# Performance work log

Hardware: AMD Instinct MI355X
Metric: run time of the kernel (lower is better)

## Reference

```python
import jax, jax.numpy as jnp
import numpy as np

B, S, HID, H, D = 2, 2048, 2048, 16, 128
ROPE_THETA = 10000.0
NEG = -1e9


def _rope_tables(seq_len, dim, theta):
    inv_freq = 1.0 / (theta ** (jnp.arange(0, dim, 2, dtype=jnp.float32) / dim))
    t = jnp.arange(seq_len, dtype=jnp.float32)
    freqs = jnp.outer(t, inv_freq)                 # [S, D/2]
    emb = jnp.concatenate([freqs, freqs], axis=-1)  # [S, D]
    return jnp.cos(emb), jnp.sin(emb)


def _rotate_half(x):
    x1, x2 = jnp.split(x, 2, axis=-1)
    return jnp.concatenate([-x2, x1], axis=-1)


def setup_inputs() -> dict:
    key = jax.random.key(0)
    ks = jax.random.split(key, 12)
    hidden_states = jax.random.normal(ks[0], (B, S, HID), dtype=jnp.float32)
    Wq = jax.random.normal(ks[1], (HID, HID), dtype=jnp.float32) * 0.02
    Wk = jax.random.normal(ks[2], (HID, HID), dtype=jnp.float32) * 0.02
    Wv = jax.random.normal(ks[3], (HID, HID), dtype=jnp.float32) * 0.02
    Wo = jax.random.normal(ks[4], (HID, HID), dtype=jnp.float32) * 0.02
    bq = jnp.zeros((HID,), jnp.float32)
    bk = jnp.zeros((HID,), jnp.float32)
    bv = jnp.zeros((HID,), jnp.float32)
    beta = jax.random.normal(ks[5], (1,), dtype=jnp.float32)
    M = jax.random.normal(ks[6], (H, D, D), dtype=jnp.float32) * 0.01
    z = jax.random.uniform(ks[7], (H, D), dtype=jnp.float32) + 1.0  # strictly positive normalizer
    causal = jnp.tril(jnp.ones((S, S), dtype=bool))
    attention_mask = jnp.broadcast_to(
        jnp.where(causal, 0.0, NEG).astype(jnp.float32)[None, None], (B, 1, S, S)
    ) + jnp.zeros((B, 1, S, S), jnp.float32)
    position_ids = jnp.broadcast_to(jnp.arange(S, dtype=jnp.int32), (B, S))
    return {
        "hidden_states": hidden_states, "Wq": Wq, "bq": bq, "Wk": Wk, "bk": bk,
        "Wv": Wv, "bv": bv, "Wo": Wo, "beta": beta, "M": M, "z": z,
        "attention_mask": attention_mask, "position_ids": position_ids,
    }


def reference(hidden_states, Wq, bq, Wk, bk, Wv, bv, Wo, beta, M, z,
              attention_mask, position_ids):
    bsz, seq, hid = hidden_states.shape
    h, d = M.shape[0], M.shape[1]

    # projections (weights stored [in, out])
    q = (hidden_states @ Wq + bq).reshape(bsz, seq, h, d).transpose(0, 2, 1, 3)  # [b,h,s,d]
    k = (hidden_states @ Wk + bk).reshape(bsz, seq, h, d).transpose(0, 2, 1, 3)
    v = (hidden_states @ Wv + bv).reshape(bsz, seq, h, d).transpose(0, 2, 1, 3)

    # RoPE
    cos, sin = _rope_tables(seq, d, ROPE_THETA)          # [s, d]
    cos = cos[position_ids][:, None]                      # [b,1,s,d]
    sin = sin[position_ids][:, None]
    q = q * cos + _rotate_half(q) * sin
    k = k * cos + _rotate_half(k) * sin

    sigma = lambda x: jax.nn.elu(x) + 1.0
    sig_q = sigma(q)
    sig_k = sigma(k)

    # compressive-memory retrieval (uses pre-update M, z)
    mem_num = jnp.einsum('bhsd,hde->bhse', sig_q, M)
    mem_den = jnp.einsum('bhsd,hd->bhs', sig_q, z)
    memory_output = mem_num / mem_den[..., None]

    # memory update via outer products of feature-mapped keys and values
    M_new = M + jnp.einsum('bhsd,bhse->hde', sig_k, v)
    z_new = z + sig_k.sum(axis=(0, 2))

    # local causal attention
    scores = jnp.einsum('bhqd,bhkd->bhqk', q, k) / jnp.sqrt(jnp.float32(d))
    scores = scores + attention_mask
    attn = jax.nn.softmax(scores, axis=-1)
    attn_output = jnp.einsum('bhqk,bhkd->bhqd', attn, v)

    # gated long-term injection
    g = jax.nn.sigmoid(beta)[0]
    combined = g * memory_output + (1.0 - g) * attn_output

    combined = combined.transpose(0, 2, 1, 3).reshape(bsz, seq, h * d)
    final_output = combined @ Wo
    return (final_output, M_new, z_new)
```

## Files before the change

### kernel.cpp

```cpp
#include <hip/hip_runtime.h>


typedef float  floatx4 __attribute__((ext_vector_type(4)));
typedef __bf16 bf16x8  __attribute__((ext_vector_type(8)));

#define DEV __device__ __forceinline__

constexpr int BN  = 2;
constexpr int SS  = 2048;
constexpr int HID = 2048;
constexpr int NH  = 16;
constexpr int DD  = 128;
constexpr int BS  = BN * SS;

DEV unsigned short f2bf(float f) {
  unsigned int u = __float_as_uint(f);
  u += 0x7FFFu + ((u >> 16) & 1u);
  return (unsigned short)(u >> 16);
}
DEV float bf2f(unsigned short h) {
  return __uint_as_float(((unsigned int)h) << 16);
}
DEV float sigma_f(float x) { return x > 0.f ? x + 1.f : __expf(x); }

DEV void cp16(const unsigned short* g, unsigned short* l) {
  __builtin_amdgcn_global_load_lds(
      (const __attribute__((address_space(1))) unsigned int*)g,
      (__attribute__((address_space(3))) unsigned int*)l, 16, 0, 0);
}

DEV bf16x8 scale8(bf16x8 x, float s) {
  bf16x8 r;
  #pragma unroll
  for (int i = 0; i < 8; i++) r[i] = (__bf16)((float)x[i] * s);
  return r;
}

DEV floatx4 mfma16(bf16x8 a, bf16x8 b, floatx4 c) {
  return __builtin_amdgcn_mfma_f32_16x16x32_bf16(a, b, c, 0, 0, 0);
}

constexpr size_t WS_WOT   = 0;
constexpr size_t WS_HSB   = WS_WOT   + (size_t)HID * HID * 2;
constexpr size_t WS_WQT   = WS_HSB   + (size_t)BS  * HID * 2;
constexpr size_t WS_WKT   = WS_WQT   + (size_t)HID * HID * 2;
constexpr size_t WS_WVT   = WS_WKT   + (size_t)HID * HID * 2;
constexpr size_t WS_QB    = WS_WVT   + (size_t)HID * HID * 2;
constexpr size_t WS_KB    = WS_QB    + (size_t)BS  * HID * 2;
constexpr size_t WS_VB    = WS_KB    + (size_t)BS  * HID * 2;
constexpr size_t WS_VTB   = WS_VB    + (size_t)BS  * HID * 2;
constexpr size_t WS_ATT   = WS_VTB   + (size_t)BS  * HID * 2;
constexpr size_t WS_COMB  = WS_ATT   + (size_t)BS  * HID * 2;
constexpr size_t WS_MPART = WS_COMB  + (size_t)BS  * HID * 2;
constexpr size_t WS_ZPART = WS_MPART + (size_t)16 * NH * DD * DD * 4;
constexpr size_t WS_MTB   = WS_ZPART + (size_t)16 * NH * DD * 4;

__global__ __launch_bounds__(256) void k_prep(const float* __restrict__ hs,
                                              const float* __restrict__ Wq, const float* __restrict__ Wk,
                                              const float* __restrict__ Wv, const float* __restrict__ Wo,
                                              const float* __restrict__ M,
                                              unsigned short* __restrict__ hsb,
                                              unsigned short* tq, unsigned short* tk,
                                              unsigned short* tv, unsigned short* to_,
                                              unsigned short* __restrict__ mtb) {
  __shared__ float tile[64][65];
  const int tid = threadIdx.x;
  if (blockIdx.z == 5) {
    if (blockIdx.y >= 16 || blockIdx.x >= 4) return;
    int h = blockIdx.y;
    int d0 = (blockIdx.x & 1) * 64, e0 = (blockIdx.x >> 1) * 64;
    const float* Mh = M + (size_t)h * DD * DD;
    #pragma unroll
    for (int i = 0; i < 16; i++) {
      int idx = i * 256 + tid; int r = idx >> 6, c = idx & 63;
      tile[r][c] = Mh[(size_t)(d0 + r) * DD + e0 + c];
    }
    __syncthreads();
    #pragma unroll
    for (int i = 0; i < 16; i++) {
      int idx = i * 256 + tid; int r = idx >> 6, c = idx & 63;
      mtb[((size_t)h * DD + e0 + r) * DD + d0 + c] = f2bf(tile[c][r]);
    }
    return;
  }
  if (blockIdx.z == 4) {
    int cid = blockIdx.y * 32 + blockIdx.x;
    const float4* src = (const float4*)hs;
    ushort4* dst = (ushort4*)hsb;
    #pragma unroll
    for (int i = 0; i < 8; i++) {
      int idx = cid * 2048 + i * 256 + tid;
      float4 v = src[idx];
      ushort4 o; o.x = f2bf(v.x); o.y = f2bf(v.y); o.z = f2bf(v.z); o.w = f2bf(v.w);
      dst[idx] = o;
    }
    return;
  }
  const float* W; unsigned short* T;
  switch (blockIdx.z) {
    case 0:  W = Wq; T = tq; break;
    case 1:  W = Wk; T = tk; break;
    case 2:  W = Wv; T = tv; break;
    default: W = Wo; T = to_; break;
  }
  int k0 = blockIdx.y * 64, n0 = blockIdx.x * 64;
  #pragma unroll
  for (int i = 0; i < 16; i++) {
    int idx = i * 256 + tid; int r = idx >> 6, c = idx & 63;
    tile[r][c] = W[(size_t)(k0 + r) * HID + n0 + c];
  }
  __syncthreads();
  #pragma unroll
  for (int i = 0; i < 16; i++) {
    int idx = i * 256 + tid; int r = idx >> 6, c = idx & 63;
    T[(size_t)(n0 + r) * HID + k0 + c] = f2bf(tile[c][r]);
  }
}

constexpr int GBM = 256, GBN = 128, GBK = 32;
constexpr int NTK = HID / GBK;
constexpr int A_U    = GBM * GBK;
constexpr int SLOT_U = (GBM + GBN) * GBK;

DEV void stage_slot(const unsigned short* __restrict__ X,
                    const unsigned short* __restrict__ Wt,
                    unsigned short* slot, int m0, int n0, int k0, int tid) {
  #pragma unroll
  for (int i = 0; i < 2; i++) {
    int c = i * 512 + tid;
    int q = c >> 3, p = c & 7, t = p ^ (q & 7);
    int row = 2 * q + (t >> 2), col = k0 + ((t & 3) << 3);
    cp16(X + (size_t)(m0 + row) * HID + col, slot + c * 8);
  }
  {
    int c = tid;
    int q = c >> 3, p = c & 7, t = p ^ (q & 7);
    int row = 2 * q + (t >> 2), col = k0 + ((t & 3) << 3);
    cp16(Wt + (size_t)(n0 + row) * HID + col, slot + A_U + c * 8);
  }
}

DEV bf16x8 ldfrag(const unsigned short* base, int r, int grp) {
  int q = r >> 1;
  int p = (((r & 1) << 2) | grp) ^ (q & 7);
  return __builtin_bit_cast(bf16x8, *(const uint4*)(base + q * 64 + p * 8));
}

DEV void gemm_core(const unsigned short* __restrict__ X,
                   const unsigned short* __restrict__ Wt,
                   unsigned short* lds, int m0, int n0, floatx4 acc[4][4]) {
  const int tid = threadIdx.x;
  const int lane = tid & 63, w = tid >> 6;
  const int grp = lane >> 4, l16 = lane & 15;
  const int wm = (w >> 1) * 64, wn = (w & 1) * 64;
  #pragma unroll
  for (int i = 0; i < 4; i++)
    #pragma unroll
    for (int j = 0; j < 4; j++) acc[i][j] = floatx4{0.f, 0.f, 0.f, 0.f};
  stage_slot(X, Wt, lds,          m0, n0, 0,   tid);
  stage_slot(X, Wt, lds + SLOT_U, m0, n0, GBK, tid);
  int sl_r = 0, sl_w = 2;
  for (int t = 0; t < NTK; t++) {
    if (t + 1 < NTK) asm volatile("s_waitcnt vmcnt(3)" ::: "memory");
    else             asm volatile("s_waitcnt vmcnt(0)" ::: "memory");
    __builtin_amdgcn_s_barrier();
    asm volatile("" ::: "memory");
    if (t + 2 < NTK)
      stage_slot(X, Wt, lds + sl_w * SLOT_U, m0, n0, (t + 2) * GBK, tid);
    const unsigned short* As = lds + sl_r * SLOT_U;
    const unsigned short* Bs = As + A_U;
    bf16x8 af[4], bfr[4];
    #pragma unroll
    for (int mi = 0; mi < 4; mi++) af[mi]  = ldfrag(As, wm + mi * 16 + l16, grp);
    #pragma unroll
    for (int ni = 0; ni < 4; ni++) bfr[ni] = ldfrag(Bs, wn + ni * 16 + l16, grp);
    __builtin_amdgcn_s_setprio(1);
    #pragma unroll
    for (int mi = 0; mi < 4; mi++)
      #pragma unroll
      for (int ni = 0; ni < 4; ni++)
        acc[mi][ni] = mfma16(af[mi], bfr[ni], acc[mi][ni]);
    __builtin_amdgcn_s_setprio(0);
    asm volatile("" ::: "memory");
    sl_r = (sl_r == 2) ? 0 : sl_r + 1;
    sl_w = (sl_w == 2) ? 0 : sl_w + 1;
  }
}

__global__ __launch_bounds__(512, 4) void k_gemm_qkv(
    const unsigned short* __restrict__ Xb,
    const unsigned short* __restrict__ Wtq, const unsigned short* __restrict__ Wtk,
    const unsigned short* __restrict__ Wtv,
    const float* __restrict__ bq, const float* __restrict__ bk, const float* __restrict__ bv,
    unsigned short* __restrict__ qb, unsigned short* __restrict__ kb,
    unsigned short* __restrict__ vtb) {
  const unsigned short* Wt; const float* bias; unsigned short* out;
  switch (blockIdx.z) {
    case 0:  Wt = Wtq; bias = bq; out = qb; break;
    case 1:  Wt = Wtk; bias = bk; out = kb; break;
    default: Wt = Wtv; bias = bv; out = nullptr; break;
  }
  __shared__ __align__(16) unsigned short lds[3 * SLOT_U];
  int lin = blockIdx.y * 16 + blockIdx.x;
  lin = (lin & 7) * 32 + (lin >> 3);
  int m0 = (lin >> 4) * GBM, n0 = (lin & 15) * GBN;
  floatx4 acc[4][4];
  gemm_core(Xb, Wt, lds, m0, n0, acc);
  const int tid = threadIdx.x;
  const int lane = tid & 63, w = tid >> 6;
  const int grp = lane >> 4, l16 = lane & 15;
  const int wm = (w >> 1) * 64, wn = (w & 1) * 64;
  if (blockIdx.z == 2) {
    #pragma unroll
    for (int mi = 0; mi < 4; mi++) {
      int gr0 = m0 + wm + mi * 16;
      int bi  = gr0 >> 11;
      int ssb = (gr0 & 2047) + grp * 4;
      #pragma unroll
      for (int ni = 0; ni < 4; ni++) {
        int col = n0 + wn + ni * 16 + l16;
        float bb_ = bias[col];
        int hh = col >> 7, dd = col & 127;
        ushort4 pk;
        unsigned short* pv = (unsigned short*)&pk;
        #pragma unroll
        for (int r = 0; r < 4; r++) pv[r] = f2bf(acc[mi][ni][r] + bb_);
        *(ushort4*)(vtb + (((size_t)(bi * NH + hh)) * DD + dd) * SS + ssb) = pk;
      }
    }
    return;
  }
  __syncthreads();
  unsigned short* T = lds;
  #pragma unroll
  for (int mi = 0; mi < 4; mi++) {
    #pragma unroll
    for (int ni = 0; ni < 4; ni++) {
      int col = wn + ni * 16 + l16;
      float bb_ = bias[n0 + col];
      #pragma unroll
      for (int r = 0; r < 4; r++)
        T[(wm + mi * 16 + grp * 4 + r) * 144 + col] = f2bf(acc[mi][ni][r] + bb_);
    }
  }
  __syncthreads();
  const int hh = n0 >> 7;
  #pragma unroll
  for (int j = 0; j < 4; j++) {
    int r = j * 64 + (tid >> 3);
    int c0 = (tid & 7) * 8;
    int grow = m0 + r;
    int bi = grow >> 11, s = grow & 2047;
    bf16x8 x1 = __builtin_bit_cast(bf16x8, *(const uint4*)(T + r * 144 + c0));
    bf16x8 x2 = __builtin_bit_cast(bf16x8, *(const uint4*)(T + r * 144 + c0 + 64));
    unsigned short o1[8], o2[8];
    #pragma unroll
    for (int jj = 0; jj < 8; jj++) {
      float ang = (float)s * __expf(-(float)(c0 + jj) * (9.210340371976184f / 64.f));
      float sn, cs;
      __sincosf(ang, &sn, &cs);
      float a1 = (float)x1[jj], a2 = (float)x2[jj];
      o1[jj] = f2bf(a1 * cs - a2 * sn);
      o2[jj] = f2bf(a2 * cs + a1 * sn);
    }
    size_t base = ((size_t)(bi * NH + hh) * SS + s) * DD;
    *(uint4*)(out + base + c0)      = *(const uint4*)o1;
    *(uint4*)(out + base + c0 + 64) = *(const uint4*)o2;
  }
}

__global__ __launch_bounds__(512, 4) void k_gemm_out(const unsigned short* __restrict__ Xb,
                                                     const unsigned short* __restrict__ Wt,
                                                     float* __restrict__ outf) {
  __shared__ __align__(16) unsigned short lds[3 * SLOT_U];
  int lin = blockIdx.y * 16 + blockIdx.x;
  lin = (lin & 7) * 32 + (lin >> 3);
  int m0 = (lin >> 4) * GBM, n0 = (lin & 15) * GBN;
  floatx4 acc[4][4];
  gemm_core(Xb, Wt, lds, m0, n0, acc);
  const int lane = threadIdx.x & 63, w = threadIdx.x >> 6;
  const int grp = lane >> 4, l16 = lane & 15;
  const int wm = (w >> 1) * 64, wn = (w & 1) * 64;
  #pragma unroll
  for (int mi = 0; mi < 4; mi++)
    #pragma unroll
    for (int ni = 0; ni < 4; ni++) {
      int col = n0 + wn + ni * 16 + l16;
      #pragma unroll
      for (int r = 0; r < 4; r++) {
        int gr = m0 + wm + mi * 16 + grp * 4 + r;
        outf[(size_t)gr * HID + col] = acc[mi][ni][r];
      }
    }
}

DEV void stage_kv(const unsigned short* __restrict__ Kg,
                  const unsigned short* __restrict__ Vg,
                  unsigned short* Klb, unsigned short* Vtlb, int tid) {
  #pragma unroll
  for (int i = 0; i < 4; i++) {
    int c = i * 256 + tid;
    int kv = c >> 4, ck = c & 15;
    cp16(Kg + kv * DD + ((ck ^ (kv & 7)) << 3), Klb + c * 8);
    int dvt = c >> 3, cv = c & 7;
    cp16(Vg + (size_t)dvt * SS + ((cv ^ (dvt & 7)) << 3), Vtlb + c * 8);
  }
}

DEV void attn_update(const unsigned short* Kl, const unsigned short* Vtl,
                     unsigned short* Plw, const bf16x8* qf, floatx4* o,
                     floatx4* lacc, bool diag, int grp, int l16, int wrow) {
  const int swk = l16 & 7;
  floatx4 sacc[4];
  #pragma unroll
  for (int j = 0; j < 4; j++) sacc[j] = floatx4{0.f, 0.f, 0.f, 0.f};
  __builtin_amdgcn_s_setprio(1);
  #pragma unroll
  for (int ks = 0; ks < 4; ks++)
    #pragma unroll
    for (int j = 0; j < 4; j++) {
      bf16x8 kf = __builtin_bit_cast(bf16x8,
          *(const uint4*)(Kl + (j * 16 + l16) * 128 + (((ks * 4 + grp) ^ swk) << 3)));
      sacc[j] = __builtin_amdgcn_mfma_f32_16x16x32_bf16(qf[ks], kf, sacc[j], 0, 0, 0);
    }
  __builtin_amdgcn_s_setprio(0);
  #pragma unroll
  for (int j = 0; j < 4; j++)
    #pragma unroll
    for (int r = 0; r < 4; r++) {
      float p = (diag && (j * 16 + l16) > (wrow + grp * 4 + r)) ? 0.f : __expf(sacc[j][r]);
      Plw[(j >> 1) * 640 + (grp * 4 + r) * 40 + (j & 1) * 16 + l16] = f2bf(p);
    }
  const bf16x8 ones = __builtin_bit_cast(bf16x8,
      uint4{0x3F803F80u, 0x3F803F80u, 0x3F803F80u, 0x3F803F80u});
  __builtin_amdgcn_s_setprio(1);
  #pragma unroll
  for (int ks2 = 0; ks2 < 2; ks2++) {
    bf16x8 pf = __builtin_bit_cast(bf16x8,
        *(const uint4*)(Plw + ks2 * 640 + l16 * 40 + grp * 8));
    *lacc = __builtin_amdgcn_mfma_f32_16x16x32_bf16(pf, ones, *lacc, 0, 0, 0);
    #pragma unroll
    for (int n = 0; n < 8; n++) {
      bf16x8 vf = __builtin_bit_cast(bf16x8,
          *(const uint4*)(Vtl + (n * 16 + l16) * 64 + (((ks2 * 4 + grp) ^ swk) << 3)));
      o[n] = __builtin_amdgcn_mfma_f32_16x16x32_bf16(pf, vf, o[n], 0, 0, 0);
    }
  }
  __builtin_amdgcn_s_setprio(0);
}

__global__ __launch_bounds__(256) void k_attn(const unsigned short* __restrict__ qb,
                                              const unsigned short* __restrict__ kb,
                                              const unsigned short* __restrict__ vtb,
                                              unsigned short* __restrict__ attb) {
  const int t = blockIdx.x, bh = blockIdx.y;
  const int qtA = t, qtB = 31 - t;
  const int tid = threadIdx.x, w = tid >> 6, lane = tid & 63;
  const int grp = lane >> 4, l16 = lane & 15;
  const unsigned short* Q  = qb  + (size_t)bh * SS * DD;
  const unsigned short* K  = kb  + (size_t)bh * SS * DD;
  const unsigned short* VT = vtb + (size_t)bh * DD * SS;
  __shared__ __align__(16) unsigned short Kl[2][64 * 128];
  __shared__ __align__(16) unsigned short Vtl[2][128 * 64];
  __shared__ __align__(16) unsigned short Pl[4][1280];
  const float sc = 0.08838834764831845f;
  bf16x8 qfA[4], qfB[4];
  {
    int qrA = qtA * 64 + w * 16 + l16, qrB = qtB * 64 + w * 16 + l16;
    #pragma unroll
    for (int ks = 0; ks < 4; ks++) {
      qfA[ks] = scale8(__builtin_bit_cast(bf16x8, *(const uint4*)(Q + (size_t)qrA * DD + ks * 32 + grp * 8)), sc);
      qfB[ks] = scale8(__builtin_bit_cast(bf16x8, *(const uint4*)(Q + (size_t)qrB * DD + ks * 32 + grp * 8)), sc);
    }
  }
  floatx4 oA[8], oB[8];
  #pragma unroll
  for (int n = 0; n < 8; n++) { oA[n] = floatx4{0,0,0,0}; oB[n] = floatx4{0,0,0,0}; }
  floatx4 laccA = floatx4{0,0,0,0}, laccB = floatx4{0,0,0,0};
  stage_kv(K, VT, Kl[0], Vtl[0], tid);
  asm volatile("s_waitcnt vmcnt(0)" ::: "memory");
  __builtin_amdgcn_s_barrier();
  int cur = 0;
  for (int kt = 0; kt <= qtB; kt++) {
    asm volatile("" ::: "memory");
    if (kt < qtB)
      stage_kv(K + (size_t)(kt + 1) * 64 * DD, VT + (size_t)(kt + 1) * 64,
               Kl[cur ^ 1], Vtl[cur ^ 1], tid);
    attn_update(Kl[cur], Vtl[cur], Pl[w], qfB, oB, &laccB, kt == qtB, grp, l16, w * 16);
    if (kt <= qtA)
      attn_update(Kl[cur], Vtl[cur], Pl[w], qfA, oA, &laccA, kt == qtA, grp, l16, w * 16);
    asm volatile("" ::: "memory");
    if (kt < qtB) {
      asm volatile("s_waitcnt vmcnt(0)" ::: "memory");
      __builtin_amdgcn_s_barrier();
    }
    cur ^= 1;
  }
  #pragma unroll
  for (int r = 0; r < 4; r++) {
    float invA = 1.f / laccA[r], invB = 1.f / laccB[r];
    int rA = qtA * 64 + w * 16 + grp * 4 + r;
    int rB = qtB * 64 + w * 16 + grp * 4 + r;
    #pragma unroll
    for (int n = 0; n < 8; n++) {
      attb[(size_t)bh * SS * DD + (size_t)rA * DD + n * 16 + l16] = f2bf(oA[n][r] * invA);
      attb[(size_t)bh * SS * DD + (size_t)rB * DD + n * 16 + l16] = f2bf(oB[n][r] * invB);
    }
  }
}

__global__ __launch_bounds__(256) void k_memcomb(const unsigned short* __restrict__ qb,
                                                 const unsigned short* __restrict__ mtb,
                                                 const float* __restrict__ z,
                                                 const float* __restrict__ beta,
                                                 const unsigned short* __restrict__ attb,
                                                 unsigned short* __restrict__ comb) {
  const int st = blockIdx.x, bh = blockIdx.y;
  const int b = bh >> 4, h = bh & 15;
  const int tid = threadIdx.x, w = tid >> 6, lane = tid & 63;
  const int grp = lane >> 4, l16 = lane & 15;
  const int s0 = st * 64;
  __shared__ __align__(16) unsigned short qtl[64 * 128];
  __shared__ __align__(16) unsigned short sqt[64 * 128];
  __shared__ float zf[128];
  __shared__ float den[64];
  #pragma unroll
  for (int i = 0; i < 4; i++) {
    int c = i * 256 + tid;
    int row = c >> 4, ch = c & 15;
    cp16(qb + ((size_t)bh * SS + s0 + row) * DD + ch * 8, qtl + c * 8);
  }
  if (tid < 32) {
    #pragma unroll
    for (int j = 0; j < 4; j++) zf[tid * 4 + j] = z[h * DD + tid * 4 + j];
  }
  asm volatile("s_waitcnt vmcnt(0)" ::: "memory");
  __syncthreads();
  #pragma unroll
  for (int i = 0; i < 4; i++) {
    int c = i * 256 + tid;
    int row = c >> 4, ch = c & 15;
    bf16x8 v = __builtin_bit_cast(bf16x8, *(const uint4*)(qtl + c * 8));
    unsigned short o8[8];
    float dp = 0.f;
    #pragma unroll
    for (int j = 0; j < 8; j++) {
      float sgv = sigma_f((float)v[j]);
      dp += sgv * zf[ch * 8 + j];
      o8[j] = f2bf(sgv);
    }
    *(uint4*)(sqt + ((size_t)row * 128 + (size_t)(ch ^ (row & 15)) * 8)) =
        *(const uint4*)o8;
    #pragma unroll
    for (int msk = 1; msk < 16; msk <<= 1) dp += __shfl_xor(dp, msk, 64);
    if (l16 == 0) den[row] = dp;
  }
  __syncthreads();
  floatx4 acc[4][2];
  #pragma unroll
  for (int mi = 0; mi < 4; mi++)
    #pragma unroll
    for (int ni = 0; ni < 2; ni++) acc[mi][ni] = floatx4{0.f, 0.f, 0.f, 0.f};
  const unsigned short* Mh = mtb + (size_t)h * DD * DD;
  #pragma unroll
  for (int k = 0; k < 4; k++) {
    bf16x8 af[4], bfr[2];
    #pragma unroll
    for (int mi = 0; mi < 4; mi++)
      af[mi] = __builtin_bit_cast(bf16x8,
          *(const uint4*)(sqt + (size_t)(mi * 16 + l16) * 128 + (size_t)((k * 4 + grp) ^ l16) * 8));
    #pragma unroll
    for (int ni = 0; ni < 2; ni++)
      bfr[ni] = __builtin_bit_cast(bf16x8,
          *(const uint4*)(Mh + (size_t)(w * 32 + ni * 16 + l16) * DD + k * 32 + grp * 8));
    #pragma unroll
    for (int mi = 0; mi < 4; mi++)
      #pragma unroll
      for (int ni = 0; ni < 2; ni++)
        acc[mi][ni] = mfma16(af[mi], bfr[ni], acc[mi][ni]);
  }
  float g = 1.f / (1.f + __expf(-beta[0]));
  #pragma unroll
  for (int mi = 0; mi < 4; mi++)
    #pragma unroll
    for (int ni = 0; ni < 2; ni++) {
      int col = w * 32 + ni * 16 + l16;
      #pragma unroll
      for (int r = 0; r < 4; r++) {
        int srow = mi * 16 + grp * 4 + r;
        float mo = acc[mi][ni][r] / den[srow];
        float at = bf2f(attb[((size_t)bh * SS + s0 + srow) * DD + col]);
        comb[((size_t)(b * SS + s0 + srow)) * HID + h * DD + col] = f2bf(g * mo + (1.f - g) * at);
      }
    }
}

__global__ __launch_bounds__(256) void k_mnew(const unsigned short* __restrict__ kb,
                                              const unsigned short* __restrict__ vtb,
                                              float* __restrict__ mpart,
                                              float* __restrict__ zpart) {
  const int ch = blockIdx.x, h = blockIdx.y;
  const int tid = threadIdx.x, lane = tid & 63, w = tid >> 6;
  const int grp = lane >> 4, l16 = lane & 15;
  const int zs = tid & 31, zdg = tid >> 5;
  __shared__ __align__(16) unsigned short skT[128 * 40];
  __shared__ __align__(16) unsigned short vl[128 * 40];
  const int b = ch >> 3;
  const int sl0 = (ch & 7) * 256;
  const unsigned short* Kg = kb  + ((size_t)(b * NH + h) * SS + sl0) * DD;
  const unsigned short* Vg = vtb + (size_t)(b * NH + h) * DD * SS + sl0;
  float zacc[16];
  #pragma unroll
  for (int j = 0; j < 16; j++) zacc[j] = 0.f;
  floatx4 acc[2][8];
  #pragma unroll
  for (int i = 0; i < 2; i++)
    #pragma unroll
    for (int j = 0; j < 8; j++) acc[i][j] = floatx4{0.f, 0.f, 0.f, 0.f};
  for (int st = 0; st < 8; st++) {
    const unsigned short* kp = Kg + (size_t)(st * 32 + zs) * DD + zdg * 16;
    bf16x8 k0 = __builtin_bit_cast(bf16x8, *(const uint4*)kp);
    bf16x8 k1 = __builtin_bit_cast(bf16x8, *(const uint4*)(kp + 8));
    int c0 = tid,        e0 = c0 >> 2, q0 = c0 & 3;
    int c1 = 256 + tid,  e1 = c1 >> 2, q1 = c1 & 3;
    uint4 vr0 = *(const uint4*)(Vg + (size_t)e0 * SS + st * 32 + q0 * 8);
    uint4 vr1 = *(const uint4*)(Vg + (size_t)e1 * SS + st * 32 + q1 * 8);
    __syncthreads();
    #pragma unroll
    for (int j = 0; j < 8; j++) {
      float s0 = sigma_f((float)k0[j]);
      float s1 = sigma_f((float)k1[j]);
      zacc[j] += s0; zacc[8 + j] += s1;
      skT[(zdg * 16 + j) * 40 + zs]     = f2bf(s0);
      skT[(zdg * 16 + 8 + j) * 40 + zs] = f2bf(s1);
    }
    *(uint4*)(vl + e0 * 40 + q0 * 8) = vr0;
    *(uint4*)(vl + e1 * 40 + q1 * 8) = vr1;
    __syncthreads();
    bf16x8 af[2], bfv[8];
    #pragma unroll
    for (int ti = 0; ti < 2; ti++)
      af[ti] = __builtin_bit_cast(bf16x8,
          *(const uint4*)(skT + (w * 32 + ti * 16 + l16) * 40 + grp * 8));
    #pragma unroll
    for (int tj = 0; tj < 8; tj++)
      bfv[tj] = __builtin_bit_cast(bf16x8,
          *(const uint4*)(vl + (tj * 16 + l16) * 40 + grp * 8));
    __builtin_amdgcn_s_setprio(1);
    #pragma unroll
    for (int ti = 0; ti < 2; ti++)
      #pragma unroll
      for (int tj = 0; tj < 8; tj++)
        acc[ti][tj] = mfma16(af[ti], bfv[tj], acc[ti][tj]);
    __builtin_amdgcn_s_setprio(0);
  }
  float* mp = mpart + ((size_t)ch * NH + h) * DD * DD;
  #pragma unroll
  for (int ti = 0; ti < 2; ti++)
    #pragma unroll
    for (int tj = 0; tj < 8; tj++) {
      int d = w * 32 + ti * 16 + grp * 4;
      int e = tj * 16 + l16;
      #pragma unroll
      for (int r = 0; r < 4; r++)
        mp[(size_t)(d + r) * DD + e] = acc[ti][tj][r];
    }
  float* zp = zpart + ((size_t)ch * NH + h) * DD;
  #pragma unroll
  for (int j = 0; j < 16; j++) {
    float v = zacc[j];
    #pragma unroll
    for (int msk = 1; msk <= 16; msk <<= 1) v += __shfl_xor(v, msk, 64);
    if (zs == 0) zp[zdg * 16 + j] = v;
  }
}

__global__ __launch_bounds__(256) void k_mreduce(const float* __restrict__ M,
                                                 const float* __restrict__ mpart,
                                                 const float* __restrict__ z,
                                                 const float* __restrict__ zpart,
                                                 float* __restrict__ outM,
                                                 float* __restrict__ outz) {
  int idx = blockIdx.x * 256 + threadIdx.x;
  float s = M[idx];
  #pragma unroll
  for (int ch = 0; ch < 16; ch++) s += mpart[(size_t)ch * NH * DD * DD + idx];
  outM[idx] = s;
  if (blockIdx.x < 8) {
    int zi = blockIdx.x * 256 + threadIdx.x;
    float zs = z[zi];
    #pragma unroll
    for (int ch = 0; ch < 16; ch++) zs += zpart[(size_t)ch * NH * DD + zi];
    outz[zi] = zs;
  }
}

extern "C" void kernel_launch(void* const* d_in, const int* in_sizes, int n_in,
                              void* d_out, int out_size, void* d_ws, size_t ws_size,
                              hipStream_t stream) {
  const float* hs   = (const float*)d_in[0];
  const float* Wq   = (const float*)d_in[1];
  const float* bq   = (const float*)d_in[2];
  const float* Wk   = (const float*)d_in[3];
  const float* bk   = (const float*)d_in[4];
  const float* Wv   = (const float*)d_in[5];
  const float* bv   = (const float*)d_in[6];
  const float* Wo   = (const float*)d_in[7];
  const float* beta = (const float*)d_in[8];
  const float* M    = (const float*)d_in[9];
  const float* z    = (const float*)d_in[10];

  char* ws = (char*)d_ws;
  unsigned short* wot  = (unsigned short*)(ws + WS_WOT);
  unsigned short* hsb  = (unsigned short*)(ws + WS_HSB);
  unsigned short* wqt  = (unsigned short*)(ws + WS_WQT);
  unsigned short* wkt  = (unsigned short*)(ws + WS_WKT);
  unsigned short* wvt  = (unsigned short*)(ws + WS_WVT);
  unsigned short* qb   = (unsigned short*)(ws + WS_QB);
  unsigned short* kb   = (unsigned short*)(ws + WS_KB);
  unsigned short* vtb  = (unsigned short*)(ws + WS_VTB);
  unsigned short* attb = (unsigned short*)(ws + WS_ATT);
  unsigned short* comb = (unsigned short*)(ws + WS_COMB);
  float*          mprt = (float*)(ws + WS_MPART);
  float*          zprt = (float*)(ws + WS_ZPART);
  unsigned short* mtb  = (unsigned short*)(ws + WS_MTB);

  float* out_final = (float*)d_out;
  float* out_M = out_final + (size_t)BS * HID;
  float* out_z = out_M + NH * DD * DD;

  k_prep    <<<dim3(32, 32, 6), 256, 0, stream>>>(hs, Wq, Wk, Wv, Wo, M, hsb, wqt, wkt, wvt, wot, mtb);
  k_gemm_qkv<<<dim3(16, 16, 3), 512, 0, stream>>>(hsb, wqt, wkt, wvt, bq, bk, bv, qb, kb, vtb);
  k_attn    <<<dim3(16, 32),    256, 0, stream>>>(qb, kb, vtb, attb);
  k_memcomb <<<dim3(32, 32),    256, 0, stream>>>(qb, mtb, z, beta, attb, comb);
  k_gemm_out<<<dim3(16, 16),    512, 0, stream>>>(comb, wot, out_final);
  k_mnew    <<<dim3(16, 16),    256, 0, stream>>>(kb, vtb, mprt, zprt);
  k_mreduce <<<dim3(1024),      256, 0, stream>>>(M, mprt, z, zprt, out_M, out_z);
}
```

Before: 428.0 us.

## Fuse memory retrieval and gated combine into attention kernel epilogue

Removes the separate k_memcomb kernel and computes sigma(q)·M and sigma(q)·z with MFMA inside the attention kernel's epilogue, reusing the Q fragments already held in registers. It recovers unscaled q by multiplying the pre-scaled bf16 fragments back, then writes the gated combination straight to comb. This saves one launch and the bf16 attention-output round trip through global memory. In exchange, M is read from global memory per wave without LDS, register pressure rises, and q is quantised twice, which slightly changes precision.

Result: slower. 439.6 us (+2.7%).

```diff
diff --git a/kernel.cpp b/kernel.cpp
--- a/kernel.cpp
+++ b/kernel.cpp
@@ -349,14 +349,55 @@
   __builtin_amdgcn_s_setprio(0);
 }
 
+DEV void mem_combine(const bf16x8* qf, const floatx4* o, const floatx4& lacc,
+                     const bf16x8* zfr, const unsigned short* __restrict__ Mh,
+                     unsigned short* __restrict__ comb, float g,
+                     int b, int h, int s_base, int grp, int l16) {
+  const float isc = 11.313708498984761f;
+  bf16x8 sf[4];
+  #pragma unroll
+  for (int ks = 0; ks < 4; ks++) {
+    unsigned short t8[8];
+    #pragma unroll
+    for (int j = 0; j < 8; j++)
+      t8[j] = f2bf(sigma_f((float)qf[ks][j] * isc));
+    sf[ks] = __builtin_bit_cast(bf16x8, *(const uint4*)t8);
+  }
+  floatx4 dacc = floatx4{0.f, 0.f, 0.f, 0.f};
+  #pragma unroll
+  for (int ks = 0; ks < 4; ks++) dacc = mfma16(sf[ks], zfr[ks], dacc);
+  #pragma unroll
+  for (int n = 0; n < 8; n++) {
+    floatx4 macc = floatx4{0.f, 0.f, 0.f, 0.f};
+    #pragma unroll
+    for (int ks = 0; ks < 4; ks++) {
+      bf16x8 bf_ = __builtin_bit_cast(bf16x8,
+          *(const uint4*)(Mh + (size_t)(n * 16 + l16) * DD + ks * 32 + grp * 8));
+      macc = mfma16(sf[ks], bf_, macc);
+    }
+    #pragma unroll
+    for (int r = 0; r < 4; r++) {
+      int s = s_base + grp * 4 + r;
+      float mo = macc[r] / dacc[r];
+      float at = o[n][r] / lacc[r];
+      comb[((size_t)(b * SS + s)) * HID + h * DD + n * 16 + l16] =
+          f2bf(g * mo + (1.f - g) * at);
+    }
+  }
+}
+
 __global__ __launch_bounds__(256) void k_attn(const unsigned short* __restrict__ qb,
                                               const unsigned short* __restrict__ kb,
                                               const unsigned short* __restrict__ vtb,
-                                              unsigned short* __restrict__ attb) {
+                                              const unsigned short* __restrict__ mtb,
+                                              const float* __restrict__ zg,
+                                              const float* __restrict__ beta,
+                                              unsigned short* __restrict__ comb) {
   const int t = blockIdx.x, bh = blockIdx.y;
   const int qtA = t, qtB = 31 - t;
   const int tid = threadIdx.x, w = tid >> 6, lane = tid & 63;
   const int grp = lane >> 4, l16 = lane & 15;
+  const int b = bh >> 4, h = bh & 15;
   const unsigned short* Q  = qb  + (size_t)bh * SS * DD;
   const unsigned short* K  = kb  + (size_t)bh * SS * DD;
   const unsigned short* VT = vtb + (size_t)bh * DD * SS;
@@ -396,103 +437,19 @@
     }
     cur ^= 1;
   }
-  #pragma unroll
-  for (int r = 0; r < 4; r++) {
-    float invA = 1.f / laccA[r], invB = 1.f / laccB[r];
-    int rA = qtA * 64 + w * 16 + grp * 4 + r;
-    int rB = qtB * 64 + w * 16 + grp * 4 + r;
-    #pragma unroll
-    for (int n = 0; n < 8; n++) {
-      attb[(size_t)bh * SS * DD + (size_t)rA * DD + n * 16 + l16] = f2bf(oA[n][r] * invA);
-      attb[(size_t)bh * SS * DD + (size_t)rB * DD + n * 16 + l16] = f2bf(oB[n][r] * invB);
-    }
-  }
-}
-
-__global__ __launch_bounds__(256) void k_memcomb(const unsigned short* __restrict__ qb,
-                                                 const unsigned short* __restrict__ mtb,
-                                                 const float* __restrict__ z,
-                                                 const float* __restrict__ beta,
-                                                 const unsigned short* __restrict__ attb,
-                                                 unsigned short* __restrict__ comb) {
-  const int st = blockIdx.x, bh = blockIdx.y;
-  const int b = bh >> 4, h = bh & 15;
-  const int tid = threadIdx.x, w = tid >> 6, lane = tid & 63;
-  const int grp = lane >> 4, l16 = lane & 15;
-  const int s0 = st * 64;
-  __shared__ __align__(16) unsigned short qtl[64 * 128];
-  __shared__ __align__(16) unsigned short sqt[64 * 128];
-  __shared__ float zf[128];
-  __shared__ float den[64];
-  #pragma unroll
-  for (int i = 0; i < 4; i++) {
-    int c = i * 256 + tid;
-    int row = c >> 4, ch = c & 15;
-    cp16(qb + ((size_t)bh * SS + s0 + row) * DD + ch * 8, qtl + c * 8);
-  }
-  if (tid < 32) {
-    #pragma unroll
-    for (int j = 0; j < 4; j++) zf[tid * 4 + j] = z[h * DD + tid * 4 + j];
-  }
-  asm volatile("s_waitcnt vmcnt(0)" ::: "memory");
-  __syncthreads();
-  #pragma unroll
-  for (int i = 0; i < 4; i++) {
-    int c = i * 256 + tid;
-    int row = c >> 4, ch = c & 15;
-    bf16x8 v = __builtin_bit_cast(bf16x8, *(const uint4*)(qtl + c * 8));
-    unsigned short o8[8];
-    float dp = 0.f;
-    #pragma unroll
-    for (int j = 0; j < 8; j++) {
-      float sgv = sigma_f((float)v[j]);
-      dp += sgv * zf[ch * 8 + j];
-      o8[j] = f2bf(sgv);
-    }
-    *(uint4*)(sqt + ((size_t)row * 128 + (size_t)(ch ^ (row & 15)) * 8)) =
-        *(const uint4*)o8;
-    #pragma unroll
-    for (int msk = 1; msk < 16; msk <<= 1) dp += __shfl_xor(dp, msk, 64);
-    if (l16 == 0) den[row] = dp;
-  }
-  __syncthreads();
-  floatx4 acc[4][2];
-  #pragma unroll
-  for (int mi = 0; mi < 4; mi++)
-    #pragma unroll
-    for (int ni = 0; ni < 2; ni++) acc[mi][ni] = floatx4{0.f, 0.f, 0.f, 0.f};
   const unsigned short* Mh = mtb + (size_t)h * DD * DD;
-  #pragma unroll
-  for (int k = 0; k < 4; k++) {
-    bf16x8 af[4], bfr[2];
-    #pragma unroll
-    for (int mi = 0; mi < 4; mi++)
-      af[mi] = __builtin_bit_cast(bf16x8,
-          *(const uint4*)(sqt + (size_t)(mi * 16 + l16) * 128 + (size_t)((k * 4 + grp) ^ l16) * 8));
-    #pragma unroll
-    for (int ni = 0; ni < 2; ni++)
-      bfr[ni] = __builtin_bit_cast(bf16x8,
-          *(const uint4*)(Mh + (size_t)(w * 32 + ni * 16 + l16) * DD + k * 32 + grp * 8));
-    #pragma unroll
-    for (int mi = 0; mi < 4; mi++)
-      #pragma unroll
-      for (int ni = 0; ni < 2; ni++)
-        acc[mi][ni] = mfma16(af[mi], bfr[ni], acc[mi][ni]);
-  }
   float g = 1.f / (1.f + __expf(-beta[0]));
-  #pragma unroll
-  for (int mi = 0; mi < 4; mi++)
-    #pragma unroll
-    for (int ni = 0; ni < 2; ni++) {
-      int col = w * 32 + ni * 16 + l16;
-      #pragma unroll
-      for (int r = 0; r < 4; r++) {
-        int srow = mi * 16 + grp * 4 + r;
-        float mo = acc[mi][ni][r] / den[srow];
-        float at = bf2f(attb[((size_t)bh * SS + s0 + srow) * DD + col]);
-        comb[((size_t)(b * SS + s0 + srow)) * HID + h * DD + col] = f2bf(g * mo + (1.f - g) * at);
-      }
-    }
+  bf16x8 zfr[4];
+  #pragma unroll
+  for (int ks = 0; ks < 4; ks++) {
+    unsigned short zt[8];
+    #pragma unroll
+    for (int j = 0; j < 8; j++)
+      zt[j] = f2bf(zg[h * DD + ks * 32 + grp * 8 + j]);
+    zfr[ks] = __builtin_bit_cast(bf16x8, *(const uint4*)zt);
+  }
+  mem_combine(qfB, oB, laccB, zfr, Mh, comb, g, b, h, qtB * 64 + w * 16, grp, l16);
+  mem_combine(qfA, oA, laccA, zfr, Mh, comb, g, b, h, qtA * 64 + w * 16, grp, l16);
 }
 
 __global__ __launch_bounds__(256) void k_mnew(const unsigned short* __restrict__ kb,
@@ -619,7 +576,6 @@
   unsigned short* qb   = (unsigned short*)(ws + WS_QB);
   unsigned short* kb   = (unsigned short*)(ws + WS_KB);
   unsigned short* vtb  = (unsigned short*)(ws + WS_VTB);
-  unsigned short* attb = (unsigned short*)(ws + WS_ATT);
   unsigned short* comb = (unsigned short*)(ws + WS_COMB);
   float*          mprt = (float*)(ws + WS_MPART);
   float*          zprt = (float*)(ws + WS_ZPART);
@@ -631,8 +587,7 @@
 
   k_prep    <<<dim3(32, 32, 6), 256, 0, stream>>>(hs, Wq, Wk, Wv, Wo, M, hsb, wqt, wkt, wvt, wot, mtb);
   k_gemm_qkv<<<dim3(16, 16, 3), 512, 0, stream>>>(hsb, wqt, wkt, wvt, bq, bk, bv, qb, kb, vtb);
-  k_attn    <<<dim3(16, 32),    256, 0, stream>>>(qb, kb, vtb, attb);
-  k_memcomb <<<dim3(32, 32),    256, 0, stream>>>(qb, mtb, z, beta, attb, comb);
+  k_attn    <<<dim3(16, 32),    256, 0, stream>>>(qb, kb, vtb, mtb, z, beta, comb);
   k_gemm_out<<<dim3(16, 16),    512, 0, stream>>>(comb, wot, out_final);
   k_mnew    <<<dim3(16, 16),    256, 0, stream>>>(kb, vtb, mprt, zprt);
   k_mreduce <<<dim3(1024),      256, 0, stream>>>(M, mprt, z, zprt, out_M, out_z);
```
